# Kernel tuning notes

Measured on AMD Instinct MI355X. Metric: run time of the kernel, lower is better.

## Reference

```python
import jax, jax.numpy as jnp
import numpy as np

B, NQ, NKV, D, H = 2, 2048, 2048, 2048, 16
HD = D // H


def setup_inputs() -> dict:
    key = jax.random.key(0)
    ks = jax.random.split(key, 9)
    return {
        "x": jax.random.normal(ks[0], (B, NQ, D), jnp.float32),
        "k": jax.random.normal(ks[1], (B, H, NKV, HD), jnp.float32),
        "v": jax.random.normal(ks[2], (B, H, NKV, HD), jnp.float32),
        "tier_labels": jax.random.randint(ks[3], (B, NKV), 0, 3),
        "padding_mask": jnp.zeros((B, NKV), dtype=bool),
        "q_w": jax.random.normal(ks[4], (D, D), jnp.float32) * (D ** -0.5),
        "q_b": jax.random.normal(ks[5], (D,), jnp.float32) * 0.02,
        "out_w": jax.random.normal(ks[6], (D, D), jnp.float32) * (D ** -0.5),
        "out_b": jax.random.normal(ks[7], (D,), jnp.float32) * 0.02,
        "tier_bias": jax.random.normal(ks[8], (3,), jnp.float32) * 0.1,
    }


def reference(x, k, v, tier_labels, padding_mask, q_w, q_b, out_w, out_b, tier_bias):
    b, n_q, d = x.shape
    h, n_kv, hd = k.shape[1], k.shape[2], k.shape[3]
    scale = hd ** -0.5
    # q projection: torch Linear is x @ W.T + b
    q = x @ q_w.T + q_b                         # [b, n_q, d]
    q = q.reshape(b, n_q, h, hd).transpose(0, 2, 1, 3)  # [b, h, n_q, hd]
    attn = jnp.einsum("bhqd,bhkd->bhqk", q, k) * scale  # [b, h, n_q, n_kv]
    # additive tier bias gathered per kv token
    attn = attn + tier_bias[tier_labels][:, None, None, :]
    # causal mask: triu(-inf, diagonal=n_kv - n_q + 1)
    causal = jnp.triu(jnp.full((n_q, n_kv), -jnp.inf, dtype=x.dtype), k=n_kv - n_q + 1)
    attn = attn + causal
    # padding mask -> -inf
    attn = jnp.where(padding_mask[:, None, None, :], -jnp.inf, attn)
    attn = jax.nn.softmax(attn, axis=-1)
    out = jnp.einsum("bhqk,bhkd->bhqd", attn, v)  # [b, h, n_q, hd]
    out = out.transpose(0, 2, 1, 3).reshape(b, n_q, d)
    return out @ out_w.T + out_b
```

## Files before the change

### kernel.cpp

```cpp
#include <hip/hip_runtime.h>
#include <stdint.h>

typedef unsigned short u16;
typedef __attribute__((ext_vector_type(8))) short short8;
typedef __attribute__((ext_vector_type(4))) float f32x4;
typedef __attribute__((ext_vector_type(4))) uint32_t u32x4;

#define B_   2
#define NQ_  2048
#define NKV_ 2048
#define D_   2048
#define H_   16
#define HD_  128
#define MM_  (B_*NQ_)
#define LOG2E 1.4426950408889634f
#define QSCALE (0.08838834764831845f * 1.4426950408889634f)

__device__ __forceinline__ u16 f2bf(float f) {
  uint32_t u = __float_as_uint(f);
  u += 0x7fffu + ((u >> 16) & 1u);
  return (u16)(u >> 16);
}

__device__ __forceinline__ void gload_lds16(const void* g, void* l) {
  __builtin_amdgcn_global_load_lds(
      (const __attribute__((address_space(1))) void*)g,
      (__attribute__((address_space(3))) void*)l, 16, 0, 0);
}

__global__ __launch_bounds__(256) void cast_bf16(const float* __restrict__ src,
                                                 u16* __restrict__ dst, int n8) {
  int i = blockIdx.x * 256 + threadIdx.x;
  if (i >= n8) return;
  const float4* s = (const float4*)src + (size_t)i * 2;
  float4 a = s[0], b = s[1];
  short8 o;
  o[0] = (short)f2bf(a.x); o[1] = (short)f2bf(a.y);
  o[2] = (short)f2bf(a.z); o[3] = (short)f2bf(a.w);
  o[4] = (short)f2bf(b.x); o[5] = (short)f2bf(b.y);
  o[6] = (short)f2bf(b.z); o[7] = (short)f2bf(b.w);
  *((short8*)dst + i) = o;
}

__global__ __launch_bounds__(256) void build_bias(const int* __restrict__ labels,
                                                  const unsigned char* __restrict__ mask,
                                                  const float* __restrict__ tb,
                                                  float* __restrict__ out, int n) {
  int i = blockIdx.x * 256 + threadIdx.x;
  if (i < n) out[i] = mask[i] ? -1e30f : tb[labels[i]] * LOG2E;
}

template<int OUT_BF16>
__global__ __launch_bounds__(256, 2) void gemm_bt(
    const u16* __restrict__ A, const u16* __restrict__ W,
    const float* __restrict__ bias, void* __restrict__ Cout,
    int M, int N, int K, float escale)
{
  __shared__ u16 As[128 * 64];
  __shared__ u16 Bs[128 * 64];
  const int tid = threadIdx.x;
  const int w = tid >> 6, l = tid & 63;
  const int lr = l & 15, lg = l >> 4;
  const int nbn = N >> 7;
  const int nwg = gridDim.x;
  int bid = blockIdx.x;
  int swz = (bid & 7) * (nwg >> 3) + (bid >> 3);
  const int bm = swz / nbn, bn = swz % nbn;
  const int wm = w >> 1, wn = w & 1;

  f32x4 acc[4][4] = {};

  const int sr = w * 32 + (l >> 3);
  const int sc = l & 7;

  for (int kt = 0; kt < K; kt += 64) {
#pragma unroll
    for (int i = 0; i < 4; ++i) {
      int r = sr + i * 8;
      int gc = kt + ((sc ^ (r & 7)) << 3);
      gload_lds16(A + (size_t)(bm * 128 + r) * K + gc, (char*)As + (w * 32 + i * 8) * 128);
      gload_lds16(W + (size_t)(bn * 128 + r) * K + gc, (char*)Bs + (w * 32 + i * 8) * 128);
    }
    __syncthreads();
#pragma unroll
    for (int ks = 0; ks < 2; ++ks) {
      short8 av[4], bv[4];
#pragma unroll
      for (int mf = 0; mf < 4; ++mf) {
        int row = wm * 64 + mf * 16 + lr;
        int pch = (ks * 4 + lg) ^ (row & 7);
        av[mf] = *(const short8*)((const char*)As + row * 128 + pch * 16);
      }
#pragma unroll
      for (int nf = 0; nf < 4; ++nf) {
        int row = wn * 64 + nf * 16 + lr;
        int pch = (ks * 4 + lg) ^ (row & 7);
        bv[nf] = *(const short8*)((const char*)Bs + row * 128 + pch * 16);
      }
#pragma unroll
      for (int mf = 0; mf < 4; ++mf)
#pragma unroll
        for (int nf = 0; nf < 4; ++nf)
          acc[mf][nf] = __builtin_amdgcn_mfma_f32_16x16x32_bf16(av[mf], bv[nf], acc[mf][nf], 0, 0, 0);
    }
    __syncthreads();
  }

  const int row0 = bm * 128 + wm * 64;
  const int col0 = bn * 128 + wn * 64;
#pragma unroll
  for (int nf = 0; nf < 4; ++nf) {
    int col = col0 + nf * 16 + lr;
    float bb = bias[col];
#pragma unroll
    for (int mf = 0; mf < 4; ++mf) {
#pragma unroll
      for (int r = 0; r < 4; ++r) {
        size_t row = (size_t)(row0 + mf * 16 + lg * 4 + r);
        float vv = (acc[mf][nf][r] + bb) * escale;
        if (OUT_BF16) ((u16*)Cout)[row * N + col] = f2bf(vv);
        else          ((float*)Cout)[row * N + col] = vv;
      }
    }
  }
}

__device__ __forceinline__ void softmax16(
    const f32x4 s[4], const f32x4 bias4[4], bool diag, int qrow, int kv0,
    int lr, int lg, float& m, float& d, f32x4 o[8], short8 ap[2])
{
  float sv[4][4];
  float pm = -3e38f;
#pragma unroll
  for (int nf = 0; nf < 4; ++nf)
#pragma unroll
    for (int r = 0; r < 4; ++r) {
      float v = s[nf][r] + bias4[nf][r];
      if (diag) {
        int kv = kv0 + nf * 16 + lg * 4 + r;
        if (kv > qrow) v = -1e30f;
      }
      sv[nf][r] = v;
      pm = fmaxf(pm, v);
    }
  pm = fmaxf(pm, __shfl_xor(pm, 16));
  pm = fmaxf(pm, __shfl_xor(pm, 32));
  float mn = fmaxf(m, pm);
  float al = __builtin_exp2f(m - mn);
  m = mn;
  float ps = 0.f;
  uint32_t pk0[4], pk1[4];
#pragma unroll
  for (int nf = 0; nf < 4; ++nf) {
    float p0 = __builtin_exp2f(sv[nf][0] - mn);
    float p1 = __builtin_exp2f(sv[nf][1] - mn);
    float p2 = __builtin_exp2f(sv[nf][2] - mn);
    float p3 = __builtin_exp2f(sv[nf][3] - mn);
    ps += (p0 + p1) + (p2 + p3);
    pk0[nf] = (uint32_t)f2bf(p0) | ((uint32_t)f2bf(p1) << 16);
    pk1[nf] = (uint32_t)f2bf(p2) | ((uint32_t)f2bf(p3) << 16);
  }
  ps += __shfl_xor(ps, 16);
  ps += __shfl_xor(ps, 32);
  d = d * al + ps;
  float alr[4];
#pragma unroll
  for (int r = 0; r < 4; ++r) alr[r] = __shfl(al, lg * 4 + r);
#pragma unroll
  for (int nf = 0; nf < 8; ++nf) {
    o[nf][0] *= alr[0]; o[nf][1] *= alr[1];
    o[nf][2] *= alr[2]; o[nf][3] *= alr[3];
  }
#pragma unroll
  for (int ks = 0; ks < 2; ++ks) {
    uint32_t rr[4];
#pragma unroll
    for (int i = 0; i < 4; ++i) {
      uint32_t c0 = ((lg & 1) == (i >> 1)) ? pk0[2 * ks] : pk0[2 * ks + 1];
      uint32_t c1 = ((lg & 1) == (i >> 1)) ? pk1[2 * ks] : pk1[2 * ks + 1];
      uint32_t contrib = (i & 1) ? c1 : c0;
      int srclg = (lg & 1) * 2 + ((i >> 1) ^ (lg >> 1));
      rr[i] = (uint32_t)__shfl((int)contrib, lr + 16 * srclg);
    }
    u32x4 t4;
    t4[0] = (lg & 2) ? rr[2] : rr[0];
    t4[1] = (lg & 2) ? rr[3] : rr[1];
    t4[2] = (lg & 2) ? rr[0] : rr[2];
    t4[3] = (lg & 2) ? rr[1] : rr[3];
    ap[ks] = __builtin_bit_cast(short8, t4);
  }
}

template<int WA>
__device__ __forceinline__ void compute_tile(
    const u16* __restrict__ ksb, const u16* __restrict__ vtb,
    const short8 aqB[4], const short8 aqA[4],
    f32x4 oB[8], f32x4 oA[8],
    float& mB, float& dB, float& mA, float& dA,
    const f32x4 bias4[4], bool diagB, bool diagA,
    int qrowB, int qrowA, int kv0, int lr, int lg)
{
  f32x4 sB[4] = {}, sA[4] = {};
  __builtin_amdgcn_s_setprio(1);
#pragma unroll
  for (int nf = 0; nf < 4; ++nf) {
#pragma unroll
    for (int ks = 0; ks < 4; ++ks) {
      int row = nf * 16 + lr;
      int pch = (ks * 4 + lg) ^ (row & 7);
      short8 bk = *(const short8*)((const char*)ksb + row * 256 + pch * 16);
      sB[nf] = __builtin_amdgcn_mfma_f32_16x16x32_bf16(bk, aqB[ks], sB[nf], 0, 0, 0);
      if (WA) sA[nf] = __builtin_amdgcn_mfma_f32_16x16x32_bf16(bk, aqA[ks], sA[nf], 0, 0, 0);
    }
  }
  __builtin_amdgcn_s_setprio(0);

  short8 apB[2], apA[2];
  softmax16(sB, bias4, diagB, qrowB, kv0, lr, lg, mB, dB, oB, apB);
  if (WA) softmax16(sA, bias4, diagA, qrowA, kv0, lr, lg, mA, dA, oA, apA);

  __builtin_amdgcn_s_setprio(1);
#pragma unroll
  for (int ks = 0; ks < 2; ++ks) {
#pragma unroll
    for (int nf = 0; nf < 8; ++nf) {
      short8 bv = *(const short8*)((const char*)vtb + (nf * 16 + lr) * 144 + ks * 64 + lg * 16);
      oB[nf] = __builtin_amdgcn_mfma_f32_16x16x32_bf16(apB[ks], bv, oB[nf], 0, 0, 0);
      if (WA) oA[nf] = __builtin_amdgcn_mfma_f32_16x16x32_bf16(apA[ks], bv, oA[nf], 0, 0, 0);
    }
  }
  __builtin_amdgcn_s_setprio(0);
}

__global__ __launch_bounds__(256, 2) void attn_fwd(
    const u16* __restrict__ Q, const u16* __restrict__ Kg,
    const u16* __restrict__ Vg, const float* __restrict__ biaskv,
    u16* __restrict__ AO)
{
  __shared__ u16 Ks[2][64 * 128];
  __shared__ u16 Vt[2][128 * 72];

  const int tid = threadIdx.x;
  const int w = tid >> 6, l = tid & 63;
  const int lr = l & 15, lg = l >> 4;

  const int bid = blockIdx.x;
  const int bh = bid & 31, pi = bid >> 5;
  const int b = bh >> 4, h = bh & 15;
  const int qtA = pi, qtB = 31 - pi;

  const size_t kvbase = ((size_t)bh) * NKV_ * HD_;
  const u16* Kh = Kg + kvbase;
  const u16* Vh = Vg + kvbase;
  const float* bkv = biaskv + b * NKV_;

  const int q0A = qtA * 64 + w * 16;
  const int q0B = qtB * 64 + w * 16;

  short8 aqA[4], aqB[4];
  {
    const u16* qpA = Q + (size_t)(b * NQ_ + q0A + lr) * D_ + h * HD_ + lg * 8;
    const u16* qpB = Q + (size_t)(b * NQ_ + q0B + lr) * D_ + h * HD_ + lg * 8;
#pragma unroll
    for (int ks = 0; ks < 4; ++ks) {
      aqA[ks] = *(const short8*)(qpA + ks * 32);
      aqB[ks] = *(const short8*)(qpB + ks * 32);
    }
  }

  f32x4 oA[8] = {}, oB[8] = {};
  float mA = -1e30f, mB = -1e30f, dA = 0.f, dB = 0.f;

  short8 vv[4];
  {
#pragma unroll
    for (int i = 0; i < 4; ++i) {
      int r = w * 16 + i * 4 + lg;
      int c = lr ^ (r & 7);
      gload_lds16(Kh + (size_t)r * HD_ + c * 8, (char*)&Ks[0][0] + (w * 16 + i * 4) * 256);
    }
    const u16* vp = Vh + (size_t)l * HD_ + w * 32;
#pragma unroll
    for (int j = 0; j < 4; ++j) vv[j] = *(const short8*)(vp + j * 8);
#pragma unroll
    for (int j = 0; j < 4; ++j)
#pragma unroll
      for (int e = 0; e < 8; ++e)
        Vt[0][(w * 32 + j * 8 + e) * 72 + l] = (u16)vv[j][e];
  }
  __syncthreads();

  int cur = 0;
  for (int kvt = 0; kvt <= qtB; ++kvt) {
    const int kv0 = kvt * 64;
    const bool haveNext = (kvt < qtB);
    if (haveNext) {
      const int kvn = kv0 + 64;
#pragma unroll
      for (int i = 0; i < 4; ++i) {
        int r = w * 16 + i * 4 + lg;
        int c = lr ^ (r & 7);
        gload_lds16(Kh + (size_t)(kvn + r) * HD_ + c * 8,
                    (char*)&Ks[cur ^ 1][0] + (w * 16 + i * 4) * 256);
      }
      const u16* vp = Vh + (size_t)(kvn + l) * HD_ + w * 32;
#pragma unroll
      for (int j = 0; j < 4; ++j) vv[j] = *(const short8*)(vp + j * 8);
    }

    f32x4 bias4[4];
#pragma unroll
    for (int nf = 0; nf < 4; ++nf)
      bias4[nf] = *(const f32x4*)(bkv + kv0 + nf * 16 + lg * 4);

    if (kvt <= qtA)
      compute_tile<1>(&Ks[cur][0], &Vt[cur][0], aqB, aqA, oB, oA, mB, dB, mA, dA,
                      bias4, kvt == qtB, kvt == qtA, q0B + lr, q0A + lr, kv0, lr, lg);
    else
      compute_tile<0>(&Ks[cur][0], &Vt[cur][0], aqB, aqA, oB, oA, mB, dB, mA, dA,
                      bias4, kvt == qtB, false, q0B + lr, q0A + lr, kv0, lr, lg);

    if (haveNext) {
#pragma unroll
      for (int j = 0; j < 4; ++j)
#pragma unroll
        for (int e = 0; e < 8; ++e)
          Vt[cur ^ 1][(w * 32 + j * 8 + e) * 72 + l] = (u16)vv[j][e];
    }
    __syncthreads();
    cur ^= 1;
  }

  float dvB[4], dvA[4];
#pragma unroll
  for (int r = 0; r < 4; ++r) {
    dvB[r] = __shfl(dB, lg * 4 + r);
    dvA[r] = __shfl(dA, lg * 4 + r);
  }
#pragma unroll
  for (int r = 0; r < 4; ++r) {
    float inv = 1.f / dvB[r];
    size_t row = (size_t)(b * NQ_ + q0B + lg * 4 + r);
#pragma unroll
    for (int nf = 0; nf < 8; ++nf)
      AO[row * D_ + h * HD_ + nf * 16 + lr] = f2bf(oB[nf][r] * inv);
  }
#pragma unroll
  for (int r = 0; r < 4; ++r) {
    float inv = 1.f / dvA[r];
    size_t row = (size_t)(b * NQ_ + q0A + lg * 4 + r);
#pragma unroll
    for (int nf = 0; nf < 8; ++nf)
      AO[row * D_ + h * HD_ + nf * 16 + lr] = f2bf(oA[nf][r] * inv);
  }
}

extern "C" void kernel_launch(void* const* d_in, const int* in_sizes, int n_in,
                              void* d_out, int out_size, void* d_ws, size_t ws_size,
                              hipStream_t stream) {
  const float* x     = (const float*)d_in[0];
  const float* k     = (const float*)d_in[1];
  const float* v     = (const float*)d_in[2];
  const int*   labels = (const int*)d_in[3];
  const unsigned char* mask = (const unsigned char*)d_in[4];
  const float* q_w   = (const float*)d_in[5];
  const float* q_b   = (const float*)d_in[6];
  const float* out_w = (const float*)d_in[7];
  const float* out_b = (const float*)d_in[8];
  const float* tbias = (const float*)d_in[9];

  char* ws = (char*)d_ws;
  u16* x_bf  = (u16*)(ws + 0);
  u16* qw_bf = (u16*)(ws + 16777216);
  u16* ow_bf = (u16*)(ws + 25165824);
  u16* k_bf  = (u16*)(ws + 33554432);
  u16* v_bf  = (u16*)(ws + 50331648);
  u16* q_bf  = (u16*)(ws + 67108864);
  u16* ao_bf = (u16*)(ws + 83886080);
  float* bkv = (float*)(ws + 100663296);

  cast_bf16<<<4096, 256, 0, stream>>>(x,     x_bf,  1048576);
  cast_bf16<<<2048, 256, 0, stream>>>(q_w,   qw_bf,  524288);
  cast_bf16<<<2048, 256, 0, stream>>>(out_w, ow_bf,  524288);
  cast_bf16<<<4096, 256, 0, stream>>>(k,     k_bf,  1048576);
  cast_bf16<<<4096, 256, 0, stream>>>(v,     v_bf,  1048576);
  build_bias<<<16, 256, 0, stream>>>(labels, mask, tbias, bkv, B_ * NKV_);

  gemm_bt<1><<<512, 256, 0, stream>>>(x_bf, qw_bf, q_b, (void*)q_bf, MM_, D_, D_, QSCALE);
  attn_fwd<<<512, 256, 0, stream>>>(q_bf, k_bf, v_bf, bkv, ao_bf);
  gemm_bt<0><<<512, 256, 0, stream>>>(ao_bf, ow_bf, out_b, d_out, MM_, D_, D_, 1.0f);
}
```

Before: 398.1 us.

## Double-buffer GEMM, lazy softmax rescale, swizzle V tile, fuse cast kernels

Merges five cast launches into one kernel, and adds double-buffered LDS staging to the projection GEMM so global loads overlap MFMA work. In attention, the running max and output are rescaled only when the new max exceeds the old by more than 8 (log2 domain), and probabilities are packed with the hardware bf16 pack instruction. The transposed V tile drops its padded stride for an XOR-swizzled layout. The cost is doubled GEMM LDS use and slightly different numerics from deferred rescaling.

```diff
diff --git a/kernel.cpp b/kernel.cpp
--- a/kernel.cpp
+++ b/kernel.cpp
@@ -22,24 +22,40 @@
   return (u16)(u >> 16);
 }
 
+__device__ __forceinline__ uint32_t cvtpk(float lo, float hi) {
+  uint32_t r;
+  asm("v_cvt_pk_bf16_f32 %0, %1, %2" : "=v"(r) : "v"(lo), "v"(hi));
+  return r;
+}
+
 __device__ __forceinline__ void gload_lds16(const void* g, void* l) {
   __builtin_amdgcn_global_load_lds(
       (const __attribute__((address_space(1))) void*)g,
       (__attribute__((address_space(3))) void*)l, 16, 0, 0);
 }
 
-__global__ __launch_bounds__(256) void cast_bf16(const float* __restrict__ src,
-                                                 u16* __restrict__ dst, int n8) {
+__global__ __launch_bounds__(256) void cast_all(
+    const float* __restrict__ x,  const float* __restrict__ qw,
+    const float* __restrict__ ow, const float* __restrict__ k,
+    const float* __restrict__ v,
+    u16* __restrict__ xo, u16* __restrict__ qwo, u16* __restrict__ owo,
+    u16* __restrict__ ko, u16* __restrict__ vo)
+{
   int i = blockIdx.x * 256 + threadIdx.x;
-  if (i >= n8) return;
-  const float4* s = (const float4*)src + (size_t)i * 2;
-  float4 a = s[0], b = s[1];
+  const float* s; u16* d; int off;
+  if      (i < 1048576) { s = x;  d = xo;  off = i; }
+  else if (i < 1572864) { s = qw; d = qwo; off = i - 1048576; }
+  else if (i < 2097152) { s = ow; d = owo; off = i - 1572864; }
+  else if (i < 3145728) { s = k;  d = ko;  off = i - 2097152; }
+  else                  { s = v;  d = vo;  off = i - 3145728; }
+  const float4* sp = (const float4*)s + (size_t)off * 2;
+  float4 a = sp[0], b = sp[1];
   short8 o;
   o[0] = (short)f2bf(a.x); o[1] = (short)f2bf(a.y);
   o[2] = (short)f2bf(a.z); o[3] = (short)f2bf(a.w);
   o[4] = (short)f2bf(b.x); o[5] = (short)f2bf(b.y);
   o[6] = (short)f2bf(b.z); o[7] = (short)f2bf(b.w);
-  *((short8*)dst + i) = o;
+  *((short8*)d + off) = o;
 }
 
 __global__ __launch_bounds__(256) void build_bias(const int* __restrict__ labels,
@@ -56,8 +72,8 @@
     const float* __restrict__ bias, void* __restrict__ Cout,
     int M, int N, int K, float escale)
 {
-  __shared__ u16 As[128 * 64];
-  __shared__ u16 Bs[128 * 64];
+  __shared__ u16 As[2][128 * 64];
+  __shared__ u16 Bs[2][128 * 64];
   const int tid = threadIdx.x;
   const int w = tid >> 6, l = tid & 63;
   const int lr = l & 15, lg = l >> 4;
@@ -73,15 +89,19 @@
   const int sr = w * 32 + (l >> 3);
   const int sc = l & 7;
 
-  for (int kt = 0; kt < K; kt += 64) {
+  auto stage = [&](int buf, int kt) {
 #pragma unroll
     for (int i = 0; i < 4; ++i) {
       int r = sr + i * 8;
       int gc = kt + ((sc ^ (r & 7)) << 3);
-      gload_lds16(A + (size_t)(bm * 128 + r) * K + gc, (char*)As + (w * 32 + i * 8) * 128);
-      gload_lds16(W + (size_t)(bn * 128 + r) * K + gc, (char*)Bs + (w * 32 + i * 8) * 128);
-    }
-    __syncthreads();
+      gload_lds16(A + (size_t)(bm * 128 + r) * K + gc,
+                  (char*)&As[buf][0] + (w * 32 + i * 8) * 128);
+      gload_lds16(W + (size_t)(bn * 128 + r) * K + gc,
+                  (char*)&Bs[buf][0] + (w * 32 + i * 8) * 128);
+    }
+  };
+
+  auto compute = [&](int buf) {
 #pragma unroll
     for (int ks = 0; ks < 2; ++ks) {
       short8 av[4], bv[4];
@@ -89,13 +109,13 @@
       for (int mf = 0; mf < 4; ++mf) {
         int row = wm * 64 + mf * 16 + lr;
         int pch = (ks * 4 + lg) ^ (row & 7);
-        av[mf] = *(const short8*)((const char*)As + row * 128 + pch * 16);
+        av[mf] = *(const short8*)((const char*)&As[buf][0] + row * 128 + pch * 16);
       }
 #pragma unroll
       for (int nf = 0; nf < 4; ++nf) {
         int row = wn * 64 + nf * 16 + lr;
         int pch = (ks * 4 + lg) ^ (row & 7);
-        bv[nf] = *(const short8*)((const char*)Bs + row * 128 + pch * 16);
+        bv[nf] = *(const short8*)((const char*)&Bs[buf][0] + row * 128 + pch * 16);
       }
 #pragma unroll
       for (int mf = 0; mf < 4; ++mf)
@@ -103,8 +123,19 @@
         for (int nf = 0; nf < 4; ++nf)
           acc[mf][nf] = __builtin_amdgcn_mfma_f32_16x16x32_bf16(av[mf], bv[nf], acc[mf][nf], 0, 0, 0);
     }
+  };
+
+  stage(0, 0);
+  __syncthreads();
+  int cur = 0;
+  const int NT = K >> 6;
+  for (int t = 0; t < NT - 1; ++t) {
+    stage(cur ^ 1, (t + 1) << 6);
+    compute(cur);
     __syncthreads();
-  }
+    cur ^= 1;
+  }
+  compute(cur);
 
   const int row0 = bm * 128 + wm * 64;
   const int col0 = bn * 128 + wn * 64;
@@ -145,32 +176,35 @@
     }
   pm = fmaxf(pm, __shfl_xor(pm, 16));
   pm = fmaxf(pm, __shfl_xor(pm, 32));
-  float mn = fmaxf(m, pm);
-  float al = __builtin_exp2f(m - mn);
-  m = mn;
+  if (__any(pm > m + 8.f)) {
+    float mn = fmaxf(m, pm);
+    float al = __builtin_exp2f(m - mn);
+    m = mn;
+    d *= al;
+    float alr[4];
+#pragma unroll
+    for (int r = 0; r < 4; ++r) alr[r] = __shfl(al, lg * 4 + r);
+#pragma unroll
+    for (int nf = 0; nf < 8; ++nf) {
+      o[nf][0] *= alr[0]; o[nf][1] *= alr[1];
+      o[nf][2] *= alr[2]; o[nf][3] *= alr[3];
+    }
+  }
   float ps = 0.f;
   uint32_t pk0[4], pk1[4];
 #pragma unroll
   for (int nf = 0; nf < 4; ++nf) {
-    float p0 = __builtin_exp2f(sv[nf][0] - mn);
-    float p1 = __builtin_exp2f(sv[nf][1] - mn);
-    float p2 = __builtin_exp2f(sv[nf][2] - mn);
-    float p3 = __builtin_exp2f(sv[nf][3] - mn);
+    float p0 = __builtin_exp2f(sv[nf][0] - m);
+    float p1 = __builtin_exp2f(sv[nf][1] - m);
+    float p2 = __builtin_exp2f(sv[nf][2] - m);
+    float p3 = __builtin_exp2f(sv[nf][3] - m);
     ps += (p0 + p1) + (p2 + p3);
-    pk0[nf] = (uint32_t)f2bf(p0) | ((uint32_t)f2bf(p1) << 16);
-    pk1[nf] = (uint32_t)f2bf(p2) | ((uint32_t)f2bf(p3) << 16);
+    pk0[nf] = cvtpk(p0, p1);
+    pk1[nf] = cvtpk(p2, p3);
   }
   ps += __shfl_xor(ps, 16);
   ps += __shfl_xor(ps, 32);
-  d = d * al + ps;
-  float alr[4];
-#pragma unroll
-  for (int r = 0; r < 4; ++r) alr[r] = __shfl(al, lg * 4 + r);
-#pragma unroll
-  for (int nf = 0; nf < 8; ++nf) {
-    o[nf][0] *= alr[0]; o[nf][1] *= alr[1];
-    o[nf][2] *= alr[2]; o[nf][3] *= alr[3];
-  }
+  d += ps;
 #pragma unroll
   for (int ks = 0; ks < 2; ++ks) {
     uint32_t rr[4];
@@ -224,7 +258,8 @@
   for (int ks = 0; ks < 2; ++ks) {
 #pragma unroll
     for (int nf = 0; nf < 8; ++nf) {
-      short8 bv = *(const short8*)((const char*)vtb + (nf * 16 + lr) * 144 + ks * 64 + lg * 16);
+      int rowv = nf * 16 + lr;
+      short8 bv = *(const short8*)(vtb + rowv * 64 + (((ks * 4 + lg) ^ (lr & 7)) << 3));
       oB[nf] = __builtin_amdgcn_mfma_f32_16x16x32_bf16(apB[ks], bv, oB[nf], 0, 0, 0);
       if (WA) oA[nf] = __builtin_amdgcn_mfma_f32_16x16x32_bf16(apA[ks], bv, oA[nf], 0, 0, 0);
     }
@@ -238,7 +273,7 @@
     u16* __restrict__ AO)
 {
   __shared__ u16 Ks[2][64 * 128];
-  __shared__ u16 Vt[2][128 * 72];
+  __shared__ u16 Vt[2][128 * 64];
 
   const int tid = threadIdx.x;
   const int w = tid >> 6, l = tid & 63;
@@ -285,8 +320,10 @@
 #pragma unroll
     for (int j = 0; j < 4; ++j)
 #pragma unroll
-      for (int e = 0; e < 8; ++e)
-        Vt[0][(w * 32 + j * 8 + e) * 72 + l] = (u16)vv[j][e];
+      for (int e = 0; e < 8; ++e) {
+        int row = w * 32 + j * 8 + e;
+        Vt[0][row * 64 + (((l >> 3) ^ (row & 7)) << 3) + (l & 7)] = (u16)vv[j][e];
+      }
   }
   __syncthreads();
 
@@ -324,8 +361,10 @@
 #pragma unroll
       for (int j = 0; j < 4; ++j)
 #pragma unroll
-        for (int e = 0; e < 8; ++e)
-          Vt[cur ^ 1][(w * 32 + j * 8 + e) * 72 + l] = (u16)vv[j][e];
+        for (int e = 0; e < 8; ++e) {
+          int row = w * 32 + j * 8 + e;
+          Vt[cur ^ 1][row * 64 + (((l >> 3) ^ (row & 7)) << 3) + (l & 7)] = (u16)vv[j][e];
+        }
     }
     __syncthreads();
     cur ^= 1;
@@ -379,11 +418,8 @@
   u16* ao_bf = (u16*)(ws + 83886080);
   float* bkv = (float*)(ws + 100663296);
 
-  cast_bf16<<<4096, 256, 0, stream>>>(x,     x_bf,  1048576);
-  cast_bf16<<<2048, 256, 0, stream>>>(q_w,   qw_bf,  524288);
-  cast_bf16<<<2048, 256, 0, stream>>>(out_w, ow_bf,  524288);
-  cast_bf16<<<4096, 256, 0, stream>>>(k,     k_bf,  1048576);
-  cast_bf16<<<4096, 256, 0, stream>>>(v,     v_bf,  1048576);
+  cast_all<<<16384, 256, 0, stream>>>(x, q_w, out_w, k, v,
+                                      x_bf, qw_bf, ow_bf, k_bf, v_bf);
   build_bias<<<16, 256, 0, stream>>>(labels, mask, tbias, bkv, B_ * NKV_);
 
   gemm_bt<1><<<512, 256, 0, stream>>>(x_bf, qw_bf, q_b, (void*)q_bf, MM_, D_, D_, QSCALE);
```

Measured after the change: 391.5 us. No clear change (-1.7%).
